# Kernel optimization log

Measured on AMD Instinct MI355X. Metric: run time of the kernel, lower is better.

Reference implementation:

```python
import jax, jax.numpy as jnp
import numpy as np
from jax import lax

B, T, U, H, INNER, V = 4, 200, 100, 320, 512, 1000
BLANK = 0


def setup_inputs() -> dict:
    key = jax.random.key(0)
    ks = jax.random.split(key, 8)
    enc_state = jax.random.normal(ks[0], (B, T, H), dtype=jnp.float32)
    dec_state = jax.random.normal(ks[1], (B, U + 1, H), dtype=jnp.float32)
    tokens = jax.random.randint(ks[2], (B, U), 1, V, dtype=jnp.int32)
    output_length = jnp.full((B,), T, dtype=jnp.int32)
    tokens_length = jnp.full((B,), U, dtype=jnp.int32)
    s1 = 1.0 / np.sqrt(2 * H)
    s2 = 1.0 / np.sqrt(INNER)
    W1 = jax.random.uniform(ks[3], (2 * H, INNER), minval=-s1, maxval=s1, dtype=jnp.float32)
    b1 = jax.random.uniform(ks[4], (INNER,), minval=-s1, maxval=s1, dtype=jnp.float32)
    W2 = jax.random.uniform(ks[5], (INNER, V), minval=-s2, maxval=s2, dtype=jnp.float32)
    b2 = jax.random.uniform(ks[6], (V,), minval=-s2, maxval=s2, dtype=jnp.float32)
    return {"enc_state": enc_state, "dec_state": dec_state, "tokens": tokens,
            "output_length": output_length, "tokens_length": tokens_length,
            "W1": W1, "b1": b1, "W2": W2, "b2": b2}


def joint_logits(enc_state, dec_state, W1, b1, W2, b2):
    # concat joint: cat(enc[b,t], dec[b,u]) @ W1 == enc @ W1[:H] + dec @ W1[H:]
    h_enc = jnp.einsum('bth,hi->bti', enc_state, W1[:H])      # (B,T,INNER)
    h_dec = jnp.einsum('buh,hi->bui', dec_state, W1[H:])      # (B,U+1,INNER)
    h = jnp.tanh(h_enc[:, :, None, :] + h_dec[:, None, :, :] + b1)  # (B,T,U+1,INNER)
    return jnp.einsum('btui,iv->btuv', h, W2) + b2            # (B,T,U+1,V)


def rnnt_loss(log_probs, tokens, output_length, tokens_length):
    # log_probs: (B,T,U+1,V); tokens: (B,U) int
    Bn, Tn, U1, _ = log_probs.shape
    blank_lp = log_probs[..., BLANK]                           # (B,T,U+1)
    label_lp = jnp.take_along_axis(
        log_probs[:, :, :U1 - 1, :],
        tokens[:, None, :, None].astype(jnp.int32).repeat(Tn, axis=1),
        axis=-1)[..., 0]                                       # (B,T,U)

    # row t=0: alpha[0,u] = sum_{u'<u} label_lp[0,u']
    def row0_step(c, a):
        n = c + a
        return n, n
    init0 = jnp.zeros((Bn,), dtype=log_probs.dtype)
    _, rest0 = lax.scan(row0_step, init0, label_lp[:, 0, :].T)  # (U,B)
    alpha0 = jnp.concatenate([init0[None], rest0], axis=0).T    # (B,U+1)

    def t_step(alpha_prev, xs):
        blank_prev, label_t = xs                # (B,U+1), (B,U)
        b = alpha_prev + blank_prev             # blank transition from row t-1
        def u_step(c, inp):
            b_u, a_prev = inp
            n = jnp.logaddexp(b_u, c + a_prev)
            return n, n
        first = b[:, 0]
        _, rest = lax.scan(u_step, first, (b[:, 1:].T, label_t.T))
        alpha_t = jnp.concatenate([first[None], rest], axis=0).T
        return alpha_t, alpha_t

    xs = (blank_lp[:, :-1, :].transpose(1, 0, 2), label_lp[:, 1:, :].transpose(1, 0, 2))
    _, alphas = lax.scan(t_step, alpha0, xs)                    # (T-1,B,U+1)
    alpha = jnp.concatenate([alpha0[None], alphas], axis=0).transpose(1, 0, 2)  # (B,T,U+1)

    bidx = jnp.arange(Bn)
    t_idx = output_length - 1
    u_idx = tokens_length
    ll = alpha[bidx, t_idx, u_idx] + blank_lp[bidx, t_idx, u_idx]
    return -jnp.mean(ll)


def reference(enc_state, dec_state, tokens, output_length, tokens_length, W1, b1, W2, b2):
    logits = joint_logits(enc_state, dec_state, W1, b1, W2, b2)
    log_probs = jax.nn.log_softmax(logits, axis=-1)
    return rnnt_loss(log_probs, tokens, output_length, tokens_length)
```

## Files before the change

### kernel.cpp

```cpp
#include <hip/hip_runtime.h>
#include <hip/hip_bf16.h>

#define T_DIM 200
#define U_DIM 100
#define U1    101
#define H_DIM 320
#define K_INNER 512
#define V_DIM 1000
#define B_DIM 4
#define ND 300
#define ROWS 48
#define XPITCH 520
#define CHUNK 8

typedef unsigned short ushort_t;
typedef unsigned char uchar_t;
typedef unsigned int uint32;
typedef long lfrag;

typedef float ffrag4 __attribute__((ext_vector_type(4)));

#define LOG2E   1.4426950408889634f
#define LOG2E16 (1.4426950408889634f * 0.0625f)
#define LN2     0.6931471805599453f

__device__ __forceinline__ float tanh_fast(float x) {
  float e = __expf(2.0f * x);
  return 1.0f - __fdividef(2.0f, e + 1.0f);
}

__device__ __forceinline__ uint2 pk_fp8x8(float t0, float t1, float t2, float t3,
                                          float t4, float t5, float t6, float t7) {
  uint2 r;
  r.x = (uint32)__builtin_amdgcn_cvt_pk_fp8_f32(t0, t1, 0, false);
  r.x = (uint32)__builtin_amdgcn_cvt_pk_fp8_f32(t2, t3, (int)r.x, true);
  r.y = (uint32)__builtin_amdgcn_cvt_pk_fp8_f32(t4, t5, 0, false);
  r.y = (uint32)__builtin_amdgcn_cvt_pk_fp8_f32(t6, t7, (int)r.y, true);
  return r;
}

__device__ __forceinline__ float dpp_up1(float v, float oldv) {
  return __int_as_float(__builtin_amdgcn_update_dpp(
      __float_as_int(oldv), __float_as_int(v), 0x138, 0xf, 0xf, false));
}

__global__ __launch_bounds__(512)
void prep_kernel(const float* __restrict__ enc, const float* __restrict__ dec,
                 const float* __restrict__ W1, const float* __restrict__ W2,
                 float* __restrict__ hEnc, float* __restrict__ hDec,
                 uchar_t* __restrict__ W2f8)
{
  __shared__ union { float sIn[8][H_DIM]; float sW[8][1024]; } sh;
  const int tid = threadIdx.x;
  const int blk = blockIdx.x;

  if (blk < 151) {
    const float* inp; float* outp; int nRows, rowOff, b0;
    if (blk < 100) { inp = enc; outp = hEnc; nRows = B_DIM * T_DIM; rowOff = 0;     b0 = blk; }
    else           { inp = dec; outp = hDec; nRows = B_DIM * U1;    rowOff = H_DIM; b0 = blk - 100; }
    const int r0 = b0 * 8;
    for (int i = tid; i < 8 * H_DIM; i += 512) {
      int r = i / H_DIM, k = i - r * H_DIM;
      int rr = r0 + r;
      sh.sIn[r][k] = (rr < nRows) ? inp[(size_t)rr * H_DIM + k] : 0.0f;
    }
    __syncthreads();
    const int c = tid;
    float acc[8];
#pragma unroll
    for (int r = 0; r < 8; ++r) acc[r] = 0.0f;
    const float* Wp = W1 + (size_t)rowOff * K_INNER + c;
    for (int k = 0; k < H_DIM; k += 4) {
      float w0 = Wp[(size_t)(k + 0) * K_INNER];
      float w1 = Wp[(size_t)(k + 1) * K_INNER];
      float w2 = Wp[(size_t)(k + 2) * K_INNER];
      float w3 = Wp[(size_t)(k + 3) * K_INNER];
#pragma unroll
      for (int r = 0; r < 8; ++r) {
        float4 s = *(const float4*)&sh.sIn[r][k];
        acc[r] = fmaf(s.w, w3, fmaf(s.z, w2, fmaf(s.y, w1, fmaf(s.x, w0, acc[r]))));
      }
    }
#pragma unroll
    for (int r = 0; r < 8; ++r) {
      int rr = r0 + r;
      if (rr < nRows) outp[(size_t)rr * K_INNER + c] = acc[r];
    }
  } else {
    const int kc = blk - 151;
    for (int i = tid; i < 8 * 1024; i += 512) {
      int r = i >> 10, n = i & 1023;
      sh.sW[r][n] = (n < V_DIM) ? W2[(size_t)(kc * 8 + r) * V_DIM + n] : 0.0f;
    }
    __syncthreads();
    const int ks = kc >> 2, q = kc & 3;
#pragma unroll
    for (int h = 0; h < 2; ++h) {
      int n = tid + h * 512;
      uint2 pk = pk_fp8x8(sh.sW[0][n] * 16.f, sh.sW[1][n] * 16.f,
                          sh.sW[2][n] * 16.f, sh.sW[3][n] * 16.f,
                          sh.sW[4][n] * 16.f, sh.sW[5][n] * 16.f,
                          sh.sW[6][n] * 16.f, sh.sW[7][n] * 16.f);
      const int ct = n >> 8, w = (n >> 6) & 3, col = n & 63;
      const size_t off = (size_t)(ct * 16 + ks) * 8192 + w * 2048 + q * 512 + col * 8;
      *(uint2*)&W2f8[off] = pk;
    }
  }
}

__global__ __launch_bounds__(256, 3)
void joint_kernel(const float* __restrict__ hEnc, const float* __restrict__ hDec,
                  const float* __restrict__ b1, const uchar_t* __restrict__ W2f8,
                  const float* __restrict__ b2, const int* __restrict__ tokens,
                  float* __restrict__ pD)
{
  __shared__ union SU {
    uchar_t X[ROWS * XPITCH];
    float red[4][ROWS][4];
  } sh;
  __shared__ __align__(16) uchar_t sB[4][2][2048];

  const int tid = threadIdx.x;
  const int b  = blockIdx.z;
  const int t0 = blockIdx.y * 12;
  const int u0 = blockIdx.x * 4;
  const int wave = tid >> 6;
  const int lane = tid & 63;
  const int l15 = lane & 15;
  const int quad = lane >> 4;

  float b2s[4][4];
#pragma unroll
  for (int ct = 0; ct < 4; ++ct)
#pragma unroll
    for (int cb = 0; cb < 4; ++cb) {
      int v = ct * 256 + wave * 64 + cb * 16 + l15;
      b2s[ct][cb] = (v < V_DIM) ? b2[v] * LOG2E : -1e30f;
    }
  int tokv[4];
#pragma unroll
  for (int j = 0; j < 4; ++j)
    tokv[j] = (u0 + j < U_DIM) ? tokens[b * U_DIM + u0 + j] : -1;

  for (int i = tid; i < ROWS * 64; i += 256) {
    const int row = i >> 6;
    const int G = i & 63;
    const int tcl = min(t0 + (row >> 2), T_DIM - 1);
    const int ucl = min(u0 + (row & 3), U1 - 1);
    const float* er = hEnc + (size_t)(b * T_DIM + tcl) * K_INNER;
    const float* dr = hDec + (size_t)(b * U1 + ucl) * K_INNER;
    const int k = G << 3;
    float4 e0 = *(const float4*)(er + k);
    float4 e1 = *(const float4*)(er + k + 4);
    float4 d0 = *(const float4*)(dr + k);
    float4 d1 = *(const float4*)(dr + k + 4);
    float4 c0 = *(const float4*)(b1 + k);
    float4 c1 = *(const float4*)(b1 + k + 4);
    uint2 pk = pk_fp8x8(tanh_fast(e0.x + d0.x + c0.x), tanh_fast(e0.y + d0.y + c0.y),
                        tanh_fast(e0.z + d0.z + c0.z), tanh_fast(e0.w + d0.w + c0.w),
                        tanh_fast(e1.x + d1.x + c1.x), tanh_fast(e1.y + d1.y + c1.y),
                        tanh_fast(e1.z + d1.z + c1.z), tanh_fast(e1.w + d1.w + c1.w));
    *(uint2*)&sh.X[row * XPITCH + (G << 3)] = pk;
  }
  __syncthreads();

  uchar_t* sBw = &sB[wave][0][0];
  const uchar_t* gW = W2f8 + (size_t)wave * 2048 + (size_t)lane * 16;

#define STAGE(gbase, bufv)                                                          \
  {                                                                                 \
    __builtin_amdgcn_global_load_lds(                                               \
        (const __attribute__((address_space(1))) void*)(gbase),                     \
        (__attribute__((address_space(3))) void*)(sBw + (bufv) * 2048), 16, 0, 0);  \
    __builtin_amdgcn_global_load_lds(                                               \
        (const __attribute__((address_space(1))) void*)((gbase) + 1024),            \
        (__attribute__((address_space(3))) void*)(sBw + (bufv) * 2048 + 1024), 16, 0, 0); \
  }

  STAGE(gW, 0)
  const uchar_t* gP = gW + 8192;

  const uchar_t* aB = &sh.X[l15 * XPITCH + quad * 8];
  const uchar_t* bL = sBw + quad * 512 + l15 * 8;

  float sumexp[3][4], labelA[3][4], blankV[3][4];
#pragma unroll
  for (int i = 0; i < 3; ++i)
#pragma unroll
    for (int j = 0; j < 4; ++j) { sumexp[i][j] = 0.0f; labelA[i][j] = 0.0f; blankV[i][j] = 0.0f; }

#pragma unroll 1
  for (int ct = 0; ct < 4; ++ct) {
    ffrag4 acc[3][4];
    ffrag4 zero4 = {0.0f, 0.0f, 0.0f, 0.0f};
#pragma unroll
    for (int rb = 0; rb < 3; ++rb)
#pragma unroll
      for (int cb = 0; cb < 4; ++cb) acc[rb][cb] = zero4;

#pragma unroll
    for (int ks = 0; ks < 16; ++ks) {
      if (ks < 15 || ct < 3) {
        STAGE(gP, (ks + 1) & 1)
        gP += 8192;
        asm volatile("s_waitcnt vmcnt(2)" ::: "memory");
      } else {
        asm volatile("s_waitcnt vmcnt(0)" ::: "memory");
      }
      lfrag av[3];
#pragma unroll
      for (int rb = 0; rb < 3; ++rb)
        av[rb] = *(const lfrag*)(aB + rb * (16 * XPITCH) + ks * 32);
      lfrag bv[4];
#pragma unroll
      for (int cb = 0; cb < 4; ++cb)
        bv[cb] = *(const lfrag*)(bL + (ks & 1) * 2048 + cb * 128);
#pragma unroll
      for (int rb = 0; rb < 3; ++rb)
#pragma unroll
        for (int cb = 0; cb < 4; ++cb)
          acc[rb][cb] = __builtin_amdgcn_mfma_f32_16x16x32_fp8_fp8(av[rb], bv[cb], acc[rb][cb], 0, 0, 0);
    }

#pragma unroll
    for (int cb = 0; cb < 4; ++cb) {
      const int v = ct * 256 + wave * 64 + cb * 16 + l15;
      const float bs = b2s[ct][cb];
#pragma unroll
      for (int rb = 0; rb < 3; ++rb)
#pragma unroll
        for (int reg = 0; reg < 4; ++reg) {
          float a = acc[rb][cb][reg];
          sumexp[rb][reg] += exp2f(fmaf(a, LOG2E16, bs));
          labelA[rb][reg] += (v == tokv[reg]) ? a : 0.0f;
        }
    }
    if (ct == 0 && wave == 0) {
#pragma unroll
      for (int rb = 0; rb < 3; ++rb)
#pragma unroll
        for (int reg = 0; reg < 4; ++reg) blankV[rb][reg] = acc[rb][0][reg];
    }
  }
#undef STAGE

#pragma unroll
  for (int mask = 1; mask <= 8; mask <<= 1) {
#pragma unroll
    for (int rb = 0; rb < 3; ++rb)
#pragma unroll
      for (int reg = 0; reg < 4; ++reg) {
        sumexp[rb][reg] += __shfl_xor(sumexp[rb][reg], mask, 64);
        labelA[rb][reg] += __shfl_xor(labelA[rb][reg], mask, 64);
      }
  }

  __syncthreads();
  if (l15 == 0) {
#pragma unroll
    for (int rb = 0; rb < 3; ++rb)
#pragma unroll
      for (int reg = 0; reg < 4; ++reg) {
        int row = rb * 16 + quad * 4 + reg;
        sh.red[wave][row][0] = sumexp[rb][reg];
        sh.red[wave][row][1] = blankV[rb][reg];
        sh.red[wave][row][2] = labelA[rb][reg];
      }
  }
  __syncthreads();
  if (tid < ROWS) {
    float S  = sh.red[0][tid][0] + sh.red[1][tid][0] + sh.red[2][tid][0] + sh.red[3][tid][0];
    float Bl = sh.red[0][tid][1] + sh.red[1][tid][1] + sh.red[2][tid][1] + sh.red[3][tid][1];
    float Lb = sh.red[0][tid][2] + sh.red[1][tid][2] + sh.red[2][tid][2] + sh.red[3][tid][2];
    int t = t0 + (tid >> 2);
    int u = u0 + (tid & 3);
    if (t < T_DIM && u < U1) {
      float lse2 = __log2f(S);
      int tok = (u < U_DIM) ? tokens[b * U_DIM + u] : 0;
      int d = t + u;
      size_t idx = (((size_t)b * ND + d) * 128 + u) * 2;
      pD[idx]     = fmaf(Bl, LOG2E16, b2[0]   * LOG2E) - lse2;
      pD[idx + 1] = fmaf(Lb, LOG2E16, b2[tok] * LOG2E) - lse2;
    }
  }
}

__global__ __launch_bounds__(256)
void dp_kernel(const float* __restrict__ pD,
               const int* __restrict__ outLen, const int* __restrict__ tokLen,
               float* __restrict__ outLoss)
{
  __shared__ __align__(16) float sD[4][3][CHUNK * 256];
  __shared__ float llsh[B_DIM];
  const int tid = threadIdx.x;
  const int wv = tid >> 6;
  const int lane = tid & 63;
  const float* src = pD + (size_t)wv * ND * 256;
  const int tIdx = outLen[wv] - 1;
  const int uIdx = tokLen[wv];
  const int dStar = tIdx + uIdx;
  const float NEG = -1e30f;
  const float blkStar = src[((size_t)dStar * 128 + uIdx) * 2];

  float aE = (lane == 0) ? 0.0f : NEG;
  float aO = NEG;
  float ll2 = 0.0f;
  if (dStar == 0 && lane == 0) ll2 = blkStar;

  const int uE = 2 * lane;

#define ISSUE(c, buf)                                                         \
  {                                                                           \
    const float* g_ = src + (size_t)(c) * (CHUNK * 256);                      \
    float* l_ = &sD[wv][(buf)][0];                                            \
    _Pragma("unroll")                                                         \
    for (int j_ = 0; j_ < CHUNK; ++j_)                                        \
      __builtin_amdgcn_global_load_lds(                                       \
        (const __attribute__((address_space(1))) void*)(g_ + j_ * 256 + lane * 4), \
        (__attribute__((address_space(3))) void*)(l_ + j_ * 256), 16, 0, 0);  \
  }

  ISSUE(0, 0)
  ISSUE(1, 1)
#pragma unroll 1
  for (int c = 0; c < 38; ++c) {
    { const int nc = c + 2; const int cc = nc <= 37 ? nc : 37; ISSUE(cc, nc % 3) }
    asm volatile("s_waitcnt vmcnt(16)" ::: "memory");
    const float* buf = &sD[wv][c % 3][0];
    float4 qv[CHUNK];
#pragma unroll
    for (int j = 0; j < CHUNK; ++j)
      qv[j] = *(const float4*)&buf[j * 256 + uE * 2];
#pragma unroll
    for (int j = 0; j < CHUNK; ++j) {
      const int d = c * CHUNK + 1 + j;
      float4 q = qv[j];
      float aO_up = dpp_up1(aO, NEG);
      float labUp = dpp_up1(q.w, NEG);
      float bt0 = aE + q.x, lt0 = aO_up + labUp;
      float mx0 = fmaxf(bt0, lt0), mn0 = fminf(bt0, lt0);
      float r0 = mx0 + __log2f(1.0f + exp2f(mn0 - mx0));
      int te = d - uE;
      float nE = ((uE <= U_DIM) && (te >= 0) && (te < T_DIM)) ? r0 : NEG;
      float bt1 = aO + q.z, lt1 = aE + q.y;
      float mx1 = fmaxf(bt1, lt1), mn1 = fminf(bt1, lt1);
      float r1 = mx1 + __log2f(1.0f + exp2f(mn1 - mx1));
      int to = te - 1;
      float nO = ((uE + 1 <= U_DIM) && (to >= 0) && (to < T_DIM)) ? r1 : NEG;
      aE = nE; aO = nO;
      if (d == dStar) {
        if (uIdx == uE)          ll2 = nE + blkStar;
        else if (uIdx == uE + 1) ll2 = nO + blkStar;
      }
    }
  }
#undef ISSUE

#pragma unroll
  for (int mask = 1; mask < 64; mask <<= 1) ll2 += __shfl_xor(ll2, mask, 64);
  if (lane == 0) llsh[wv] = ll2;
  __syncthreads();
  if (tid == 0)
    outLoss[0] = -(llsh[0] + llsh[1] + llsh[2] + llsh[3]) * 0.25f * LN2;
}

extern "C" void kernel_launch(void* const* d_in, const int* in_sizes, int n_in,
                              void* d_out, int out_size, void* d_ws, size_t ws_size,
                              hipStream_t stream)
{
  const float* enc    = (const float*)d_in[0];
  const float* dec    = (const float*)d_in[1];
  const int*   tokens = (const int*)d_in[2];
  const int*   outLen = (const int*)d_in[3];
  const int*   tokLen = (const int*)d_in[4];
  const float* W1     = (const float*)d_in[5];
  const float* b1     = (const float*)d_in[6];
  const float* W2     = (const float*)d_in[7];
  const float* b2     = (const float*)d_in[8];
  float* out = (float*)d_out;

  char* ws = (char*)d_ws;
  float*   hEnc = (float*)(ws + 0);
  float*   hDec = (float*)(ws + 1638400);
  uchar_t* W2f8 = (uchar_t*)(ws + 2465792);
  float*   pD   = (float*)(ws + 2990080);

  prep_kernel<<<dim3(215), dim3(512), 0, stream>>>(enc, dec, W1, W2, hEnc, hDec, W2f8);
  joint_kernel<<<dim3(26, 17, B_DIM), dim3(256), 0, stream>>>(hEnc, hDec, b1, W2f8, b2, tokens, pD);
  dp_kernel<<<dim3(1), dim3(256), 0, stream>>>(pD, outLen, tokLen, out);
}
```

Measured before the change: 257.9 us.

## Split tanh activation generation into a separate kernel and compute blank/label logits in FP32

Adds an xgen kernel that computes tanh(hEnc+hDec+b1) once per (b,t,u), writes FP8 activations to global memory in a swizzled layout, and computes blank and label logits exactly in FP32 via dot products with W2 columns. The joint kernel now only loads the precomputed activations with global_load_lds and accumulates the log-sum-exp, with the label/blank bookkeeping removed. The dp kernel combines the two buffers. This removes the duplicated tanh work across tiles and frees registers for higher occupancy, at the cost of an extra ~41MB global write and read, plus one more kernel launch.

Result: slower. 291.3 us (+13.0%).

```diff
diff --git a/kernel.cpp b/kernel.cpp
--- a/kernel.cpp
+++ b/kernel.cpp
@@ -10,7 +10,6 @@
 #define B_DIM 4
 #define ND 300
 #define ROWS 48
-#define XPITCH 520
 #define CHUNK 8
 
 typedef unsigned short ushort_t;
@@ -23,6 +22,9 @@
 #define LOG2E   1.4426950408889634f
 #define LOG2E16 (1.4426950408889634f * 0.0625f)
 #define LN2     0.6931471805599453f
+
+#define AS1 __attribute__((address_space(1)))
+#define AS3 __attribute__((address_space(3)))
 
 __device__ __forceinline__ float tanh_fast(float x) {
   float e = __expf(2.0f * x);
@@ -108,15 +110,76 @@
   }
 }
 
-__global__ __launch_bounds__(256, 3)
-void joint_kernel(const float* __restrict__ hEnc, const float* __restrict__ hDec,
-                  const float* __restrict__ b1, const uchar_t* __restrict__ W2f8,
-                  const float* __restrict__ b2, const int* __restrict__ tokens,
-                  float* __restrict__ pD)
+__global__ __launch_bounds__(256)
+void xgen_kernel(const float* __restrict__ hEnc, const float* __restrict__ hDec,
+                 const float* __restrict__ b1, const float* __restrict__ W2,
+                 const float* __restrict__ b2, const int* __restrict__ tokens,
+                 uchar_t* __restrict__ Xg, float* __restrict__ pBL)
+{
+  const int u = blockIdx.x;
+  const int b = blockIdx.y;
+  const int tid = threadIdx.x;
+  const int w = tid >> 6, lane = tid & 63;
+  const int k0 = lane * 8;
+  const int tok = (u < U_DIM) ? tokens[b * U_DIM + u] : 0;
+
+  float dR[8], wB[8], wL[8];
+  const float* dptr = hDec + (size_t)(b * U1 + u) * K_INNER + k0;
+#pragma unroll
+  for (int j = 0; j < 8; ++j) dR[j] = dptr[j] + b1[k0 + j];
+#pragma unroll
+  for (int j = 0; j < 8; ++j) {
+    wB[j] = W2[(size_t)(k0 + j) * V_DIM];
+    wL[j] = W2[(size_t)(k0 + j) * V_DIM + tok];
+  }
+  const float b2b = b2[0], b2l = b2[tok];
+  const int x7r = ((w & 1) << 2) | (u & 3);
+  const int slotoff = (lane ^ x7r) << 3;
+
+#pragma unroll 2
+  for (int i = 0; i < 50; ++i) {
+    const int t = i * 4 + w;
+    const float* er = hEnc + (size_t)(b * T_DIM + t) * K_INNER + k0;
+    float4 e0 = *(const float4*)er;
+    float4 e1 = *(const float4*)(er + 4);
+    float x0 = tanh_fast(e0.x + dR[0]);
+    float x1 = tanh_fast(e0.y + dR[1]);
+    float x2 = tanh_fast(e0.z + dR[2]);
+    float x3 = tanh_fast(e0.w + dR[3]);
+    float x4 = tanh_fast(e1.x + dR[4]);
+    float x5 = tanh_fast(e1.y + dR[5]);
+    float x6 = tanh_fast(e1.z + dR[6]);
+    float x7 = tanh_fast(e1.w + dR[7]);
+    uint2 pk = pk_fp8x8(x0, x1, x2, x3, x4, x5, x6, x7);
+    *(uint2*)&Xg[((size_t)(b * T_DIM + t) * U1 + u) * 512 + slotoff] = pk;
+    float db = x0 * wB[0];
+    db = fmaf(x1, wB[1], db); db = fmaf(x2, wB[2], db); db = fmaf(x3, wB[3], db);
+    db = fmaf(x4, wB[4], db); db = fmaf(x5, wB[5], db); db = fmaf(x6, wB[6], db);
+    db = fmaf(x7, wB[7], db);
+    float dl = x0 * wL[0];
+    dl = fmaf(x1, wL[1], dl); dl = fmaf(x2, wL[2], dl); dl = fmaf(x3, wL[3], dl);
+    dl = fmaf(x4, wL[4], dl); dl = fmaf(x5, wL[5], dl); dl = fmaf(x6, wL[6], dl);
+    dl = fmaf(x7, wL[7], dl);
+#pragma unroll
+    for (int m = 1; m < 64; m <<= 1) {
+      db += __shfl_xor(db, m, 64);
+      dl += __shfl_xor(dl, m, 64);
+    }
+    if (lane == 0) {
+      const int d = t + u;
+      float2* o = (float2*)&pBL[((size_t)(b * ND + d) * 128 + u) * 2];
+      *o = make_float2((db + b2b) * LOG2E, (dl + b2l) * LOG2E);
+    }
+  }
+}
+
+__global__ __launch_bounds__(256, 4)
+void joint_kernel(const uchar_t* __restrict__ Xg, const uchar_t* __restrict__ W2f8,
+                  const float* __restrict__ b2, float* __restrict__ pL)
 {
   __shared__ union SU {
-    uchar_t X[ROWS * XPITCH];
-    float red[4][ROWS][4];
+    uchar_t X[ROWS * 512];
+    float red[4][ROWS];
   } sh;
   __shared__ __align__(16) uchar_t sB[4][2][2048];
 
@@ -137,57 +200,42 @@
       int v = ct * 256 + wave * 64 + cb * 16 + l15;
       b2s[ct][cb] = (v < V_DIM) ? b2[v] * LOG2E : -1e30f;
     }
-  int tokv[4];
-#pragma unroll
-  for (int j = 0; j < 4; ++j)
-    tokv[j] = (u0 + j < U_DIM) ? tokens[b * U_DIM + u0 + j] : -1;
-
-  for (int i = tid; i < ROWS * 64; i += 256) {
-    const int row = i >> 6;
-    const int G = i & 63;
-    const int tcl = min(t0 + (row >> 2), T_DIM - 1);
-    const int ucl = min(u0 + (row & 3), U1 - 1);
-    const float* er = hEnc + (size_t)(b * T_DIM + tcl) * K_INNER;
-    const float* dr = hDec + (size_t)(b * U1 + ucl) * K_INNER;
-    const int k = G << 3;
-    float4 e0 = *(const float4*)(er + k);
-    float4 e1 = *(const float4*)(er + k + 4);
-    float4 d0 = *(const float4*)(dr + k);
-    float4 d1 = *(const float4*)(dr + k + 4);
-    float4 c0 = *(const float4*)(b1 + k);
-    float4 c1 = *(const float4*)(b1 + k + 4);
-    uint2 pk = pk_fp8x8(tanh_fast(e0.x + d0.x + c0.x), tanh_fast(e0.y + d0.y + c0.y),
-                        tanh_fast(e0.z + d0.z + c0.z), tanh_fast(e0.w + d0.w + c0.w),
-                        tanh_fast(e1.x + d1.x + c1.x), tanh_fast(e1.y + d1.y + c1.y),
-                        tanh_fast(e1.z + d1.z + c1.z), tanh_fast(e1.w + d1.w + c1.w));
-    *(uint2*)&sh.X[row * XPITCH + (G << 3)] = pk;
-  }
-  __syncthreads();
+
+#pragma unroll
+  for (int j = 0; j < 6; ++j) {
+    const int idx = wave * 6 + j;
+    const int tt = idx >> 1, h = idx & 1;
+    const int t = min(t0 + tt, T_DIM - 1);
+    const uchar_t* g = Xg + ((size_t)(b * T_DIM + t) * U1 + u0) * 512 + h * 1024 + (size_t)lane * 16;
+    __builtin_amdgcn_global_load_lds((const AS1 void*)g,
+                                     (AS3 void*)&sh.X[tt * 2048 + h * 1024], 16, 0, 0);
+  }
 
   uchar_t* sBw = &sB[wave][0][0];
   const uchar_t* gW = W2f8 + (size_t)wave * 2048 + (size_t)lane * 16;
-
 #define STAGE(gbase, bufv)                                                          \
   {                                                                                 \
     __builtin_amdgcn_global_load_lds(                                               \
-        (const __attribute__((address_space(1))) void*)(gbase),                     \
-        (__attribute__((address_space(3))) void*)(sBw + (bufv) * 2048), 16, 0, 0);  \
+        (const AS1 void*)(gbase),                                                   \
+        (AS3 void*)(sBw + (bufv) * 2048), 16, 0, 0);                                \
     __builtin_amdgcn_global_load_lds(                                               \
-        (const __attribute__((address_space(1))) void*)((gbase) + 1024),            \
-        (__attribute__((address_space(3))) void*)(sBw + (bufv) * 2048 + 1024), 16, 0, 0); \
-  }
-
+        (const AS1 void*)((gbase) + 1024),                                          \
+        (AS3 void*)(sBw + (bufv) * 2048 + 1024), 16, 0, 0);                         \
+  }
   STAGE(gW, 0)
   const uchar_t* gP = gW + 8192;
-
-  const uchar_t* aB = &sh.X[l15 * XPITCH + quad * 8];
+  __syncthreads();
+
+  const int x7 = l15 & 7;
+  const uchar_t* aL2 = &sh.X[l15 * 512 + ((quad ^ (x7 & 3)) << 3)];
+  const int x74s = (x7 & 4) << 3;
   const uchar_t* bL = sBw + quad * 512 + l15 * 8;
 
-  float sumexp[3][4], labelA[3][4], blankV[3][4];
+  float sumexp[3][4];
 #pragma unroll
   for (int i = 0; i < 3; ++i)
 #pragma unroll
-    for (int j = 0; j < 4; ++j) { sumexp[i][j] = 0.0f; labelA[i][j] = 0.0f; blankV[i][j] = 0.0f; }
+    for (int j = 0; j < 4; ++j) sumexp[i][j] = 0.0f;
 
 #pragma unroll 1
   for (int ct = 0; ct < 4; ++ct) {
@@ -200,21 +248,23 @@
 
 #pragma unroll
     for (int ks = 0; ks < 16; ++ks) {
-      if (ks < 15 || ct < 3) {
+      if (ct < 3 || ks < 15) {
         STAGE(gP, (ks + 1) & 1)
         gP += 8192;
         asm volatile("s_waitcnt vmcnt(2)" ::: "memory");
       } else {
         asm volatile("s_waitcnt vmcnt(0)" ::: "memory");
       }
+      const int aoff = (32 * ks) ^ x74s;
       lfrag av[3];
-#pragma unroll
-      for (int rb = 0; rb < 3; ++rb)
-        av[rb] = *(const lfrag*)(aB + rb * (16 * XPITCH) + ks * 32);
+      av[0] = *(const lfrag*)(aL2 + aoff);
+      av[1] = *(const lfrag*)(aL2 + aoff + 8192);
+      av[2] = *(const lfrag*)(aL2 + aoff + 16384);
+      const uchar_t* bk = bL + ((ks & 1) << 11);
       lfrag bv[4];
 #pragma unroll
       for (int cb = 0; cb < 4; ++cb)
-        bv[cb] = *(const lfrag*)(bL + (ks & 1) * 2048 + cb * 128);
+        bv[cb] = *(const lfrag*)(bk + cb * 128);
 #pragma unroll
       for (int rb = 0; rb < 3; ++rb)
 #pragma unroll
@@ -224,83 +274,61 @@
 
 #pragma unroll
     for (int cb = 0; cb < 4; ++cb) {
-      const int v = ct * 256 + wave * 64 + cb * 16 + l15;
       const float bs = b2s[ct][cb];
 #pragma unroll
       for (int rb = 0; rb < 3; ++rb)
 #pragma unroll
-        for (int reg = 0; reg < 4; ++reg) {
-          float a = acc[rb][cb][reg];
-          sumexp[rb][reg] += exp2f(fmaf(a, LOG2E16, bs));
-          labelA[rb][reg] += (v == tokv[reg]) ? a : 0.0f;
-        }
-    }
-    if (ct == 0 && wave == 0) {
-#pragma unroll
-      for (int rb = 0; rb < 3; ++rb)
-#pragma unroll
-        for (int reg = 0; reg < 4; ++reg) blankV[rb][reg] = acc[rb][0][reg];
+        for (int reg = 0; reg < 4; ++reg)
+          sumexp[rb][reg] += exp2f(fmaf(acc[rb][cb][reg], LOG2E16, bs));
     }
   }
 #undef STAGE
 
 #pragma unroll
-  for (int mask = 1; mask <= 8; mask <<= 1) {
+  for (int mask = 1; mask <= 8; mask <<= 1)
 #pragma unroll
     for (int rb = 0; rb < 3; ++rb)
 #pragma unroll
-      for (int reg = 0; reg < 4; ++reg) {
+      for (int reg = 0; reg < 4; ++reg)
         sumexp[rb][reg] += __shfl_xor(sumexp[rb][reg], mask, 64);
-        labelA[rb][reg] += __shfl_xor(labelA[rb][reg], mask, 64);
-      }
-  }
 
   __syncthreads();
   if (l15 == 0) {
 #pragma unroll
     for (int rb = 0; rb < 3; ++rb)
 #pragma unroll
-      for (int reg = 0; reg < 4; ++reg) {
-        int row = rb * 16 + quad * 4 + reg;
-        sh.red[wave][row][0] = sumexp[rb][reg];
-        sh.red[wave][row][1] = blankV[rb][reg];
-        sh.red[wave][row][2] = labelA[rb][reg];
-      }
+      for (int reg = 0; reg < 4; ++reg)
+        sh.red[wave][rb * 16 + quad * 4 + reg] = sumexp[rb][reg];
   }
   __syncthreads();
   if (tid < ROWS) {
-    float S  = sh.red[0][tid][0] + sh.red[1][tid][0] + sh.red[2][tid][0] + sh.red[3][tid][0];
-    float Bl = sh.red[0][tid][1] + sh.red[1][tid][1] + sh.red[2][tid][1] + sh.red[3][tid][1];
-    float Lb = sh.red[0][tid][2] + sh.red[1][tid][2] + sh.red[2][tid][2] + sh.red[3][tid][2];
+    float S = sh.red[0][tid] + sh.red[1][tid] + sh.red[2][tid] + sh.red[3][tid];
     int t = t0 + (tid >> 2);
     int u = u0 + (tid & 3);
-    if (t < T_DIM && u < U1) {
-      float lse2 = __log2f(S);
-      int tok = (u < U_DIM) ? tokens[b * U_DIM + u] : 0;
-      int d = t + u;
-      size_t idx = (((size_t)b * ND + d) * 128 + u) * 2;
-      pD[idx]     = fmaf(Bl, LOG2E16, b2[0]   * LOG2E) - lse2;
-      pD[idx + 1] = fmaf(Lb, LOG2E16, b2[tok] * LOG2E) - lse2;
-    }
+    if (t < T_DIM && u < U1)
+      pL[(size_t)(b * ND + t + u) * 128 + u] = __log2f(S);
   }
 }
 
 __global__ __launch_bounds__(256)
-void dp_kernel(const float* __restrict__ pD,
+void dp_kernel(const float* __restrict__ pBL, const float* __restrict__ pL,
                const int* __restrict__ outLen, const int* __restrict__ tokLen,
                float* __restrict__ outLoss)
 {
-  __shared__ __align__(16) float sD[4][3][CHUNK * 256];
+  __shared__ __align__(16) float sA[4][3][CHUNK * 256];
+  __shared__ __align__(16) float sL[4][3][CHUNK * 128];
   __shared__ float llsh[B_DIM];
   const int tid = threadIdx.x;
   const int wv = tid >> 6;
   const int lane = tid & 63;
-  const float* src = pD + (size_t)wv * ND * 256;
+  const float* srcA = pBL + (size_t)wv * ND * 256;
+  const float* srcL = pL  + (size_t)wv * ND * 128;
   const int tIdx = outLen[wv] - 1;
   const int uIdx = tokLen[wv];
   const int dStar = tIdx + uIdx;
   const float NEG = -1e30f;
-  const float blkStar = src[((size_t)dStar * 128 + uIdx) * 2];
+  const float blkStar = srcA[((size_t)dStar * 128 + uIdx) * 2]
+                      - srcL[(size_t)dStar * 128 + uIdx];
 
   float aE = (lane == 0) ? 0.0f : NEG;
   float aO = NEG;
@@ -309,15 +337,22 @@
 
   const int uE = 2 * lane;
 
-#define ISSUE(c, buf)                                                         \
-  {                                                                           \
-    const float* g_ = src + (size_t)(c) * (CHUNK * 256);                      \
-    float* l_ = &sD[wv][(buf)][0];                                            \
-    _Pragma("unroll")                                                         \
-    for (int j_ = 0; j_ < CHUNK; ++j_)                                        \
-      __builtin_amdgcn_global_load_lds(                                       \
-        (const __attribute__((address_space(1))) void*)(g_ + j_ * 256 + lane * 4), \
-        (__attribute__((address_space(3))) void*)(l_ + j_ * 256), 16, 0, 0);  \
+#define ISSUE(c, buf)                                                          \
+  {                                                                            \
+    const float* gA_ = srcA + (size_t)(c) * (CHUNK * 256);                     \
+    const float* gL_ = srcL + (size_t)(c) * (CHUNK * 128);                     \
+    float* lA_ = &sA[wv][(buf)][0];                                            \
+    float* lL_ = &sL[wv][(buf)][0];                                            \
+    _Pragma("unroll")                                                          \
+    for (int j_ = 0; j_ < CHUNK; ++j_)                                         \
+      __builtin_amdgcn_global_load_lds(                                        \
+        (const AS1 void*)(gA_ + j_ * 256 + lane * 4),                          \
+        (AS3 void*)(lA_ + j_ * 256), 16, 0, 0);                                \
+    _Pragma("unroll")                                                          \
+    for (int j_ = 0; j_ < 4; ++j_)                                             \
+      __builtin_amdgcn_global_load_lds(                                        \
+        (const AS1 void*)(gL_ + j_ * 256 + lane * 4),                          \
+        (AS3 void*)(lL_ + j_ * 256), 16, 0, 0);                                \
   }
 
   ISSUE(0, 0)
@@ -325,24 +360,30 @@
 #pragma unroll 1
   for (int c = 0; c < 38; ++c) {
     { const int nc = c + 2; const int cc = nc <= 37 ? nc : 37; ISSUE(cc, nc % 3) }
-    asm volatile("s_waitcnt vmcnt(16)" ::: "memory");
-    const float* buf = &sD[wv][c % 3][0];
+    asm volatile("s_waitcnt vmcnt(24)" ::: "memory");
+    const float* bufA = &sA[wv][c % 3][0];
+    const float* bufL = &sL[wv][c % 3][0];
     float4 qv[CHUNK];
-#pragma unroll
-    for (int j = 0; j < CHUNK; ++j)
-      qv[j] = *(const float4*)&buf[j * 256 + uE * 2];
+    float2 lv[CHUNK];
+#pragma unroll
+    for (int j = 0; j < CHUNK; ++j) {
+      qv[j] = *(const float4*)&bufA[j * 256 + uE * 2];
+      lv[j] = *(const float2*)&bufL[j * 128 + uE];
+    }
 #pragma unroll
     for (int j = 0; j < CHUNK; ++j) {
       const int d = c * CHUNK + 1 + j;
-      float4 q = qv[j];
+      float4 q = qv[j]; float2 lz = lv[j];
+      float BE = q.x - lz.x, LE = q.y - lz.x;
+      float BO = q.z - lz.y, LO = q.w - lz.y;
       float aO_up = dpp_up1(aO, NEG);
-      float labUp = dpp_up1(q.w, NEG);
-      float bt0 = aE + q.x, lt0 = aO_up + labUp;
+      float labUp = dpp_up1(LO, NEG);
+      float bt0 = aE + BE, lt0 = aO_up + labUp;
       float mx0 = fmaxf(bt0, lt0), mn0 = fminf(bt0, lt0);
       float r0 = mx0 + __log2f(1.0f + exp2f(mn0 - mx0));
       int te = d - uE;
       float nE = ((uE <= U_DIM) && (te >= 0) && (te < T_DIM)) ? r0 : NEG;
-      float bt1 = aO + q.z, lt1 = aE + q.y;
+      float bt1 = aO + BO, lt1 = aE + LE;
       float mx1 = fmaxf(bt1, lt1), mn1 = fminf(bt1, lt1);
       float r1 = mx1 + __log2f(1.0f + exp2f(mn1 - mx1));
       int to = te - 1;
@@ -383,9 +424,12 @@
   float*   hEnc = (float*)(ws + 0);
   float*   hDec = (float*)(ws + 1638400);
   uchar_t* W2f8 = (uchar_t*)(ws + 2465792);
-  float*   pD   = (float*)(ws + 2990080);
+  uchar_t* Xg   = (uchar_t*)(ws + 2990080);
+  float*   pBL  = (float*)(ws + 44363776);
+  float*   pL   = (float*)(ws + 45592576);
 
   prep_kernel<<<dim3(215), dim3(512), 0, stream>>>(enc, dec, W1, W2, hEnc, hDec, W2f8);
-  joint_kernel<<<dim3(26, 17, B_DIM), dim3(256), 0, stream>>>(hEnc, hDec, b1, W2f8, b2, tokens, pD);
-  dp_kernel<<<dim3(1), dim3(256), 0, stream>>>(pD, outLen, tokLen, out);
-}
+  xgen_kernel<<<dim3(101, B_DIM), dim3(256), 0, stream>>>(hEnc, hDec, b1, W2, b2, tokens, Xg, pBL);
+  joint_kernel<<<dim3(26, 17, B_DIM), dim3(256), 0, stream>>>(Xg, W2f8, b2, pL);
+  dp_kernel<<<dim3(1), dim3(256), 0, stream>>>(pBL, pL, outLen, tokLen, out);
+}
```

## Precompute fp8 tanh activations in separate kernel and stream into LDS with swizzle

Applied to the files above, without the earlier changes.

Moves the tanh(enc+dec+b1) fp8 activation generation out of the joint kernel into a new xgen kernel that writes a full (B,T,U+1,512) fp8 tensor to global memory in an XOR-swizzled layout. The joint kernel then loads its tile straight into LDS with global_load_lds, overlapped with the first W2 stage, and reads A fragments through a matching swizzle in place of the old padded pitch. The aim is to cut per-block tanh compute and its sync stall. The cost is an extra launch and a write-then-read of about 41 MB of intermediate data.

Result: slower. 264.0 us (+2.4%).

```diff
diff --git a/kernel.cpp b/kernel.cpp
--- a/kernel.cpp
+++ b/kernel.cpp
@@ -10,7 +10,6 @@
 #define B_DIM 4
 #define ND 300
 #define ROWS 48
-#define XPITCH 520
 #define CHUNK 8
 
 typedef unsigned short ushort_t;
@@ -23,6 +22,9 @@
 #define LOG2E   1.4426950408889634f
 #define LOG2E16 (1.4426950408889634f * 0.0625f)
 #define LN2     0.6931471805599453f
+
+#define AS1 __attribute__((address_space(1)))
+#define AS3 __attribute__((address_space(3)))
 
 __device__ __forceinline__ float tanh_fast(float x) {
   float e = __expf(2.0f * x);
@@ -108,14 +110,41 @@
   }
 }
 
+__global__ __launch_bounds__(256)
+void xgen_kernel(const float* __restrict__ hEnc, const float* __restrict__ hDec,
+                 const float* __restrict__ b1, uchar_t* __restrict__ Xg)
+{
+  const int gw = blockIdx.x * 4 + (threadIdx.x >> 6);
+  const int lane = threadIdx.x & 63;
+  const int b = gw / (T_DIM * U1);
+  const int rem = gw - b * (T_DIM * U1);
+  const int t = rem / U1;
+  const int u = rem - t * U1;
+  const int k0 = lane * 8;
+
+  const float* er = hEnc + (size_t)(b * T_DIM + t) * K_INNER + k0;
+  const float* dr = hDec + (size_t)(b * U1 + u) * K_INNER + k0;
+  float4 e0 = *(const float4*)er;
+  float4 e1 = *(const float4*)(er + 4);
+  float4 d0 = *(const float4*)dr;
+  float4 d1 = *(const float4*)(dr + 4);
+  float4 c0 = *(const float4*)(b1 + k0);
+  float4 c1 = *(const float4*)(b1 + k0 + 4);
+  uint2 pk = pk_fp8x8(tanh_fast(e0.x + d0.x + c0.x), tanh_fast(e0.y + d0.y + c0.y),
+                      tanh_fast(e0.z + d0.z + c0.z), tanh_fast(e0.w + d0.w + c0.w),
+                      tanh_fast(e1.x + d1.x + c1.x), tanh_fast(e1.y + d1.y + c1.y),
+                      tanh_fast(e1.z + d1.z + c1.z), tanh_fast(e1.w + d1.w + c1.w));
+  const int slotoff = (lane ^ (((t & 1) << 2) | (u & 3))) << 3;
+  *(uint2*)&Xg[((size_t)(b * T_DIM + t) * U1 + u) * 512 + slotoff] = pk;
+}
+
 __global__ __launch_bounds__(256, 3)
-void joint_kernel(const float* __restrict__ hEnc, const float* __restrict__ hDec,
-                  const float* __restrict__ b1, const uchar_t* __restrict__ W2f8,
+void joint_kernel(const uchar_t* __restrict__ Xg, const uchar_t* __restrict__ W2f8,
                   const float* __restrict__ b2, const int* __restrict__ tokens,
                   float* __restrict__ pD)
 {
   __shared__ union SU {
-    uchar_t X[ROWS * XPITCH];
+    uchar_t X[ROWS * 512];
     float red[4][ROWS][4];
   } sh;
   __shared__ __align__(16) uchar_t sB[4][2][2048];
@@ -142,45 +171,34 @@
   for (int j = 0; j < 4; ++j)
     tokv[j] = (u0 + j < U_DIM) ? tokens[b * U_DIM + u0 + j] : -1;
 
-  for (int i = tid; i < ROWS * 64; i += 256) {
-    const int row = i >> 6;
-    const int G = i & 63;
-    const int tcl = min(t0 + (row >> 2), T_DIM - 1);
-    const int ucl = min(u0 + (row & 3), U1 - 1);
-    const float* er = hEnc + (size_t)(b * T_DIM + tcl) * K_INNER;
-    const float* dr = hDec + (size_t)(b * U1 + ucl) * K_INNER;
-    const int k = G << 3;
-    float4 e0 = *(const float4*)(er + k);
-    float4 e1 = *(const float4*)(er + k + 4);
-    float4 d0 = *(const float4*)(dr + k);
-    float4 d1 = *(const float4*)(dr + k + 4);
-    float4 c0 = *(const float4*)(b1 + k);
-    float4 c1 = *(const float4*)(b1 + k + 4);
-    uint2 pk = pk_fp8x8(tanh_fast(e0.x + d0.x + c0.x), tanh_fast(e0.y + d0.y + c0.y),
-                        tanh_fast(e0.z + d0.z + c0.z), tanh_fast(e0.w + d0.w + c0.w),
-                        tanh_fast(e1.x + d1.x + c1.x), tanh_fast(e1.y + d1.y + c1.y),
-                        tanh_fast(e1.z + d1.z + c1.z), tanh_fast(e1.w + d1.w + c1.w));
-    *(uint2*)&sh.X[row * XPITCH + (G << 3)] = pk;
-  }
-  __syncthreads();
+#pragma unroll
+  for (int j = 0; j < 6; ++j) {
+    const int idx = wave * 6 + j;
+    const int tt = idx >> 1, h = idx & 1;
+    const int t = min(t0 + tt, T_DIM - 1);
+    const uchar_t* g = Xg + ((size_t)(b * T_DIM + t) * U1 + u0) * 512 + h * 1024 + (size_t)lane * 16;
+    __builtin_amdgcn_global_load_lds((const AS1 void*)g,
+                                     (AS3 void*)&sh.X[tt * 2048 + h * 1024], 16, 0, 0);
+  }
 
   uchar_t* sBw = &sB[wave][0][0];
   const uchar_t* gW = W2f8 + (size_t)wave * 2048 + (size_t)lane * 16;
-
 #define STAGE(gbase, bufv)                                                          \
   {                                                                                 \
     __builtin_amdgcn_global_load_lds(                                               \
-        (const __attribute__((address_space(1))) void*)(gbase),                     \
-        (__attribute__((address_space(3))) void*)(sBw + (bufv) * 2048), 16, 0, 0);  \
+        (const AS1 void*)(gbase),                                                   \
+        (AS3 void*)(sBw + (bufv) * 2048), 16, 0, 0);                                \
     __builtin_amdgcn_global_load_lds(                                               \
-        (const __attribute__((address_space(1))) void*)((gbase) + 1024),            \
-        (__attribute__((address_space(3))) void*)(sBw + (bufv) * 2048 + 1024), 16, 0, 0); \
-  }
-
+        (const AS1 void*)((gbase) + 1024),                                          \
+        (AS3 void*)(sBw + (bufv) * 2048 + 1024), 16, 0, 0);                         \
+  }
   STAGE(gW, 0)
   const uchar_t* gP = gW + 8192;
-
-  const uchar_t* aB = &sh.X[l15 * XPITCH + quad * 8];
+  __syncthreads();
+
+  const int x7 = l15 & 7;
+  const uchar_t* aL2 = &sh.X[l15 * 512 + ((quad ^ (x7 & 3)) << 3)];
+  const int x74s = (x7 & 4) << 3;
   const uchar_t* bL = sBw + quad * 512 + l15 * 8;
 
   float sumexp[3][4], labelA[3][4], blankV[3][4];
@@ -200,21 +218,23 @@
 
 #pragma unroll
     for (int ks = 0; ks < 16; ++ks) {
-      if (ks < 15 || ct < 3) {
+      if (ct < 3 || ks < 15) {
         STAGE(gP, (ks + 1) & 1)
         gP += 8192;
         asm volatile("s_waitcnt vmcnt(2)" ::: "memory");
       } else {
         asm volatile("s_waitcnt vmcnt(0)" ::: "memory");
       }
+      const int aoff = (32 * ks) ^ x74s;
       lfrag av[3];
-#pragma unroll
-      for (int rb = 0; rb < 3; ++rb)
-        av[rb] = *(const lfrag*)(aB + rb * (16 * XPITCH) + ks * 32);
+      av[0] = *(const lfrag*)(aL2 + aoff);
+      av[1] = *(const lfrag*)(aL2 + aoff + 8192);
+      av[2] = *(const lfrag*)(aL2 + aoff + 16384);
+      const uchar_t* bk = bL + ((ks & 1) << 11);
       lfrag bv[4];
 #pragma unroll
       for (int cb = 0; cb < 4; ++cb)
-        bv[cb] = *(const lfrag*)(bL + (ks & 1) * 2048 + cb * 128);
+        bv[cb] = *(const lfrag*)(bk + cb * 128);
 #pragma unroll
       for (int rb = 0; rb < 3; ++rb)
 #pragma unroll
@@ -245,7 +265,7 @@
 #undef STAGE
 
 #pragma unroll
-  for (int mask = 1; mask <= 8; mask <<= 1) {
+  for (int mask = 1; mask <= 8; mask <<= 1)
 #pragma unroll
     for (int rb = 0; rb < 3; ++rb)
 #pragma unroll
@@ -253,7 +273,6 @@
         sumexp[rb][reg] += __shfl_xor(sumexp[rb][reg], mask, 64);
         labelA[rb][reg] += __shfl_xor(labelA[rb][reg], mask, 64);
       }
-  }
 
   __syncthreads();
   if (l15 == 0) {
@@ -277,8 +296,7 @@
     if (t < T_DIM && u < U1) {
       float lse2 = __log2f(S);
       int tok = (u < U_DIM) ? tokens[b * U_DIM + u] : 0;
-      int d = t + u;
-      size_t idx = (((size_t)b * ND + d) * 128 + u) * 2;
+      size_t idx = (((size_t)(b * ND + t + u)) * 128 + u) * 2;
       pD[idx]     = fmaf(Bl, LOG2E16, b2[0]   * LOG2E) - lse2;
       pD[idx + 1] = fmaf(Lb, LOG2E16, b2[tok] * LOG2E) - lse2;
     }
@@ -316,8 +334,8 @@
     _Pragma("unroll")                                                         \
     for (int j_ = 0; j_ < CHUNK; ++j_)                                        \
       __builtin_amdgcn_global_load_lds(                                       \
-        (const __attribute__((address_space(1))) void*)(g_ + j_ * 256 + lane * 4), \
-        (__attribute__((address_space(3))) void*)(l_ + j_ * 256), 16, 0, 0);  \
+        (const AS1 void*)(g_ + j_ * 256 + lane * 4),                          \
+        (AS3 void*)(l_ + j_ * 256), 16, 0, 0);                                \
   }
 
   ISSUE(0, 0)
@@ -383,9 +401,11 @@
   float*   hEnc = (float*)(ws + 0);
   float*   hDec = (float*)(ws + 1638400);
   uchar_t* W2f8 = (uchar_t*)(ws + 2465792);
-  float*   pD   = (float*)(ws + 2990080);
+  uchar_t* Xg   = (uchar_t*)(ws + 2990080);
+  float*   pD   = (float*)(ws + 44363776);
 
   prep_kernel<<<dim3(215), dim3(512), 0, stream>>>(enc, dec, W1, W2, hEnc, hDec, W2f8);
-  joint_kernel<<<dim3(26, 17, B_DIM), dim3(256), 0, stream>>>(hEnc, hDec, b1, W2f8, b2, tokens, pD);
+  xgen_kernel<<<dim3(20200), dim3(256), 0, stream>>>(hEnc, hDec, b1, Xg);
+  joint_kernel<<<dim3(26, 17, B_DIM), dim3(256), 0, stream>>>(Xg, W2f8, b2, tokens, pD);
   dp_kernel<<<dim3(1), dim3(256), 0, stream>>>(pD, outLen, tokLen, out);
 }
```
